# Kernel tuning notes

Hardware: AMD Instinct MI355X
Metric: run time of the kernel (lower is better)

Reference implementation:

```python
import jax, jax.numpy as jnp
import numpy as np

B, I, H, OH = 16384, 256, 256, 64
N_STEPS = 8  # fixed-step dopri5 (adaptive step control replaced by fixed grid for jit)


def setup_inputs() -> dict:
    key = jax.random.key(0)
    ks = jax.random.split(key, 12)
    sH = 1.0 / np.sqrt(H)
    sOH = 1.0 / np.sqrt(OH)
    u = lambda k, shape, s: jax.random.uniform(k, shape, jnp.float32, -s, s)
    return {
        "input": jax.random.normal(ks[0], (B, I), jnp.float32),
        "h_prev": jax.random.normal(ks[1], (B, H), jnp.float32),
        "c_prev": jax.random.normal(ks[2], (B, H), jnp.float32),
        "timespans": jax.random.uniform(ks[3], (B,), jnp.float32, 0.05, 1.0),
        # LSTMCell params (PyTorch layout: gates stacked as [i, f, g, o])
        "W_ih": u(ks[4], (4 * H, I), sH),
        "W_hh": u(ks[5], (4 * H, H), sH),
        "b_ih": u(ks[6], (4 * H,), sH),
        "b_hh": u(ks[7], (4 * H,), sH),
        # ode_func: Linear(H, OH) -> Tanh -> Linear(OH, H)
        "W1": u(ks[8], (OH, H), sH),
        "b1": u(ks[9], (OH,), sH),
        "W2": u(ks[10], (H, OH), sOH),
        "b2": u(ks[11], (H,), sOH),
    }


def reference(input, h_prev, c_prev, timespans, W_ih, W_hh, b_ih, b_hh, W1, b1, W2, b2):
    # --- LSTMCell ---
    gates = input @ W_ih.T + b_ih + h_prev @ W_hh.T + b_hh  # (B, 4H)
    gi, gf, gg, go = jnp.split(gates, 4, axis=-1)
    i = jax.nn.sigmoid(gi)
    f = jax.nn.sigmoid(gf)
    g = jnp.tanh(gg)
    o = jax.nn.sigmoid(go)
    c = f * c_prev + i * g
    h = o * jnp.tanh(c)

    # --- Neural ODE: dy/dt = MLP(y), autonomous, Dormand-Prince RK45 ---
    def ode_f(y):
        return jnp.tanh(y @ W1.T + b1) @ W2.T + b2

    dt = (timespans / N_STEPS)[:, None]  # (B, 1) per-sample step size

    def dopri5_step(y, _):
        k1 = ode_f(y)
        k2 = ode_f(y + dt * (1.0 / 5.0 * k1))
        k3 = ode_f(y + dt * (3.0 / 40.0 * k1 + 9.0 / 40.0 * k2))
        k4 = ode_f(y + dt * (44.0 / 45.0 * k1 - 56.0 / 15.0 * k2 + 32.0 / 9.0 * k3))
        k5 = ode_f(y + dt * (19372.0 / 6561.0 * k1 - 25360.0 / 2187.0 * k2
                             + 64448.0 / 6561.0 * k3 - 212.0 / 729.0 * k4))
        k6 = ode_f(y + dt * (9017.0 / 3168.0 * k1 - 355.0 / 33.0 * k2
                             + 46732.0 / 5247.0 * k3 + 49.0 / 176.0 * k4
                             - 5103.0 / 18656.0 * k5))
        y_next = y + dt * (35.0 / 384.0 * k1 + 500.0 / 1113.0 * k3 + 125.0 / 192.0 * k4
                           - 2187.0 / 6784.0 * k5 + 11.0 / 84.0 * k6)
        return y_next, None

    h_ode, _ = jax.lax.scan(dopri5_step, h, None, length=N_STEPS)
    return h_ode, c
```

## Files before the change

kernel.cpp:

```cpp
#include <hip/hip_runtime.h>
#include <hip/hip_bf16.h>


#define B_N 16384
#define H_N 256

typedef __attribute__((ext_vector_type(8))) short short8;
typedef __attribute__((ext_vector_type(4))) unsigned short u16x4;
typedef __attribute__((ext_vector_type(4))) float f32x4;

__device__ __forceinline__ unsigned short f2bf_s(float x) {
  __hip_bfloat16 h = __float2bfloat16(x);
  return *reinterpret_cast<unsigned short*>(&h);
}

__device__ __forceinline__ short8 pack8f(const float* p) {
  const f32x4 a = *(const f32x4*)p;
  const f32x4 b = *(const f32x4*)(p + 4);
  short8 r;
  r[0] = (short)f2bf_s(a[0]); r[1] = (short)f2bf_s(a[1]);
  r[2] = (short)f2bf_s(a[2]); r[3] = (short)f2bf_s(a[3]);
  r[4] = (short)f2bf_s(b[0]); r[5] = (short)f2bf_s(b[1]);
  r[6] = (short)f2bf_s(b[2]); r[7] = (short)f2bf_s(b[3]);
  return r;
}

__device__ __forceinline__ u16x4 pack4(f32x4 v) {
  u16x4 r;
  r[0] = f2bf_s(v[0]); r[1] = f2bf_s(v[1]);
  r[2] = f2bf_s(v[2]); r[3] = f2bf_s(v[3]);
  return r;
}

__device__ __forceinline__ float fast_sigmoid(float x) {
  return __builtin_amdgcn_rcpf(1.f + __expf(-x));
}
__device__ __forceinline__ float fast_tanh(float x) {
  x = fminf(15.f, fmaxf(-15.f, x));
  float e = __expf(2.f * x);
  return 1.f - 2.f * __builtin_amdgcn_rcpf(e + 1.f);
}

__device__ __forceinline__ void gl_lds16(const void* g, void* l) {
  __builtin_amdgcn_global_load_lds(
      (const __attribute__((address_space(1))) void*)g,
      (__attribute__((address_space(3))) void*)l, 16, 0, 0);
}

__global__ __launch_bounds__(256) void prep_kernel(
    const float* __restrict__ Wih, const float* __restrict__ Whh,
    const float* __restrict__ W1, const float* __restrict__ W2,
    const float* __restrict__ b2,
    unsigned short* __restrict__ wsB, unsigned short* __restrict__ wcB,
    float* __restrict__ uF) {
  const int bx = blockIdx.x;
  if (bx < 256) {
    int idx = bx * 256 + threadIdx.x;
    int n = idx >> 6, c = idx & 63, k = c * 8;
    const float* src = (k < 256) ? (Wih + (size_t)n * 256 + k)
                                 : (Whh + (size_t)n * 256 + (k - 256));
    *(short8*)(wsB + (size_t)n * 512 + k) = pack8f(src);
  } else if (bx < 272) {
    int idx = (bx - 256) * 256 + threadIdx.x;
    int f = idx >> 6, o = idx & 63;
    float acc = 0.f;
    for (int h = 0; h < 256; ++h)
      acc = fmaf(W1[f * 256 + h], W2[h * 64 + o], acc);
    wcB[f * 64 + o] = f2bf_s(acc);
  } else {
    int f = threadIdx.x;
    if (f < 64) {
      float acc = 0.f;
      for (int h = 0; h < 256; ++h) acc = fmaf(W1[f * 256 + h], b2[h], acc);
      uF[f] = acc;
    }
  }
}

__global__ __launch_bounds__(256, 2) void lstm_kernel(
    const float* __restrict__ x, const float* __restrict__ hp,
    const float* __restrict__ cp, const unsigned short* __restrict__ wsB,
    const float* __restrict__ bih, const float* __restrict__ bhh,
    float* __restrict__ out) {
  __shared__ __align__(16) float As[128 * 64];
  __shared__ __align__(16) unsigned short Bs[256 * 64];

  const int lane = threadIdx.x & 63;
  const int wv = threadIdx.x >> 6;
  const int s = lane & 15, q = lane >> 4;
  const int mb = blockIdx.x * 128;
  const int hb = blockIdx.y * 64;

  f32x4 acc[2][16];
#pragma unroll
  for (int mt = 0; mt < 2; ++mt)
#pragma unroll
    for (int tn = 0; tn < 16; ++tn) acc[mt][tn] = (f32x4){0.f, 0.f, 0.f, 0.f};

  float bsum[16];
#pragma unroll
  for (int tn = 0; tn < 16; ++tn) {
    int n = (tn >> 2) * 256 + hb + (tn & 3) * 16 + s;
    bsum[tn] = bih[n] + bhh[n];
  }

  for (int kt8 = 0; kt8 < 8; ++kt8) {
    const int k0 = kt8 * 64;
    if (kt8) __syncthreads();
    {
      const float* srcA = (k0 < 256) ? x : hp;
      const int kl = k0 & 255;
#pragma unroll
      for (int c = 0; c < 8; ++c) {
        int row = (wv * 8 + c) * 4 + (lane >> 4);
        int uc = (lane & 15) ^ (row & 15);
        gl_lds16(srcA + (size_t)(mb + row) * 256 + kl + uc * 4,
                 (char*)As + (wv * 8 + c) * 1024);
      }
    }
#pragma unroll
    for (int c = 0; c < 8; ++c) {
      int t = (wv * 8 + c) * 8 + (lane >> 3);
      int uc = (lane & 7) ^ (t & 7);
      int gr = (t >> 6) * 256 + hb + (t & 63);
      gl_lds16(wsB + (size_t)gr * 512 + k0 + uc * 8,
               (char*)Bs + (wv * 8 + c) * 1024);
    }
    __syncthreads();

#pragma unroll
    for (int kk = 0; kk < 2; ++kk) {
      short8 af[2];
#pragma unroll
      for (int mt = 0; mt < 2; ++mt) {
        int ar = wv * 32 + mt * 16 + s;
        int c0 = kk * 8 + q * 2;
        float tmp[8];
        *(f32x4*)tmp = *(const f32x4*)((char*)As + ar * 256 + ((c0 ^ (ar & 15)) * 16));
        *(f32x4*)(tmp + 4) =
            *(const f32x4*)((char*)As + ar * 256 + (((c0 + 1) ^ (ar & 15)) * 16));
        af[mt] = pack8f(tmp);
      }
#pragma unroll
      for (int tn = 0; tn < 16; ++tn) {
        int t = (tn >> 2) * 64 + (tn & 3) * 16 + s;
        int ch = (kk * 4 + q) ^ (t & 7);
        short8 bf = *(const short8*)((char*)Bs + t * 128 + ch * 16);
        acc[0][tn] = __builtin_amdgcn_mfma_f32_16x16x32_bf16(af[0], bf, acc[0][tn], 0, 0, 0);
        acc[1][tn] = __builtin_amdgcn_mfma_f32_16x16x32_bf16(af[1], bf, acc[1][tn], 0, 0, 0);
      }
    }
  }

#pragma unroll
  for (int mt = 0; mt < 2; ++mt)
#pragma unroll
    for (int ntl = 0; ntl < 4; ++ntl)
#pragma unroll
      for (int r = 0; r < 4; ++r) {
        int sample = mb + wv * 32 + mt * 16 + q * 4 + r;
        int h = hb + ntl * 16 + s;
        float gi = acc[mt][ntl][r]      + bsum[ntl];
        float gf = acc[mt][4 + ntl][r]  + bsum[4 + ntl];
        float gg = acc[mt][8 + ntl][r]  + bsum[8 + ntl];
        float go = acc[mt][12 + ntl][r] + bsum[12 + ntl];
        float iv = fast_sigmoid(gi), fv = fast_sigmoid(gf);
        float gv = fast_tanh(gg), ov = fast_sigmoid(go);
        float c = fv * cp[(size_t)sample * 256 + h] + iv * gv;
        float hv = ov * fast_tanh(c);
        out[(size_t)B_N * H_N + (size_t)sample * 256 + h] = c;
        out[(size_t)sample * 256 + h] = hv;
      }
}

__global__ __launch_bounds__(256, 4) void ode_kernel(
    float* __restrict__ out, const float* __restrict__ ts,
    const float* __restrict__ W1, const unsigned short* __restrict__ wcB,
    const float* __restrict__ uF, const float* __restrict__ W2,
    const float* __restrict__ b1, const float* __restrict__ b2) {
  __shared__ __align__(16) unsigned short zcA[16 * 64];
  __shared__ __align__(16) unsigned short zcB2[16 * 64];
  char* zA = (char*)zcA;
  char* zB = (char*)zcB2;

  const int tid = threadIdx.x;
  const int lane = tid & 63, wv = tid >> 6;
  const int s = lane & 15, q = lane >> 4;
  const int bb = blockIdx.x * 16;
  const int sx7 = s & 7;

  short8 wcf[2];
#pragma unroll
  for (int kt = 0; kt < 2; ++kt)
    wcf[kt] = *(const short8*)(wcB + (size_t)(wv * 16 + s) * 64 + kt * 32 + q * 8);

  const f32x4 b1v = *(const f32x4*)(b1 + wv * 16 + q * 4);
  const f32x4 u4 = *(const f32x4*)(uF + wv * 16 + q * 4);
  const float dt = ts[bb + s] * 0.125f;

  f32x4 yreg[4];
#pragma unroll
  for (int i = 0; i < 4; ++i)
    yreg[i] = *(const f32x4*)(out + (size_t)(bb + s) * 256 + wv * 64 + i * 16 + q * 4);

  f32x4 G = (f32x4){0.f, 0.f, 0.f, 0.f};
#pragma unroll
  for (int kt = 0; kt < 8; ++kt) {
    short8 w1f = pack8f(W1 + (size_t)(wv * 16 + s) * 256 + kt * 32 + q * 8);
    short8 yf = pack8f(out + (size_t)(bb + s) * 256 + kt * 32 + q * 8);
    G = __builtin_amdgcn_mfma_f32_16x16x32_bf16(w1f, yf, G, 0, 0, 0);
  }

  const int zwoff = (((wv * 2 + (q >> 1)) ^ sx7) << 4) + (q & 1) * 8;
  const int rb = s * 128;

  auto stz = [&](char* buf, f32x4 v) { *(u16x4*)(buf + rb + zwoff) = pack4(v); };
  auto wcmm = [&](const char* buf) -> f32x4 {
    const char* rp = buf + rb;
    short8 zf0 = *(const short8*)(rp + ((q ^ sx7) << 4));
    short8 zf1 = *(const short8*)(rp + (((4 + q) ^ sx7) << 4));
    f32x4 a = (f32x4){0.f, 0.f, 0.f, 0.f};
    a = __builtin_amdgcn_mfma_f32_16x16x32_bf16(wcf[0], zf0, a, 0, 0, 0);
    a = __builtin_amdgcn_mfma_f32_16x16x32_bf16(wcf[1], zf1, a, 0, 0, 0);
    return a;
  };
  auto stage = [&](char* buf, f32x4 zc, float cj) -> f32x4 {
    stz(buf, zc);
    __syncthreads();
    f32x4 o = wcmm(buf);
    f32x4 zo;
#pragma unroll
    for (int r = 0; r < 4; ++r)
      zo[r] = fast_tanh(fmaf(dt, fmaf(cj, u4[r], o[r]), G[r]) + b1v[r]);
    return zo;
  };

  const float A31 = 3.f / 40.f, A32 = 9.f / 40.f;
  const float A41 = 44.f / 45.f, A42 = -56.f / 15.f, A43 = 32.f / 9.f;
  const float A51 = 19372.f / 6561.f, A52 = -25360.f / 2187.f,
              A53 = 64448.f / 6561.f, A54 = -212.f / 729.f;
  const float A61 = 9017.f / 3168.f, A62 = -355.f / 33.f, A63 = 46732.f / 5247.f,
              A64 = 49.f / 176.f, A65 = -5103.f / 18656.f;
  const float C1 = 35.f / 384.f, C3 = 500.f / 1113.f, C4 = 125.f / 192.f,
              C5 = -2187.f / 6784.f, C6 = 11.f / 84.f;

  f32x4 SC = (f32x4){0.f, 0.f, 0.f, 0.f};

  for (int st = 0; st < 8; ++st) {
    f32x4 z1;
#pragma unroll
    for (int r = 0; r < 4; ++r) z1[r] = fast_tanh(G[r] + b1v[r]);

    f32x4 z2 = stage(zA, 0.2f * z1, 0.2f);
    f32x4 z3 = stage(zB, A31 * z1 + A32 * z2, 0.3f);
    f32x4 z4 = stage(zA, A41 * z1 + A42 * z2 + A43 * z3, 0.8f);
    f32x4 z5 = stage(zB, A51 * z1 + A52 * z2 + A53 * z3 + A54 * z4, 8.f / 9.f);
    f32x4 z6 = stage(zA, A61 * z1 + A62 * z2 + A63 * z3 + A64 * z4 + A65 * z5, 1.0f);

    f32x4 zc = C1 * z1 + C3 * z3 + C4 * z4 + C5 * z5 + C6 * z6;
    stz(zB, zc);
    __syncthreads();
    f32x4 o6 = wcmm(zB);
    SC += zc;
#pragma unroll
    for (int r = 0; r < 4; ++r) G[r] = fmaf(dt, u4[r] + o6[r], G[r]);
  }

  stz(zA, SC);
  __syncthreads();
  {
    const char* rp = zA + rb;
    short8 zf0 = *(const short8*)(rp + ((q ^ sx7) << 4));
    short8 zf1 = *(const short8*)(rp + (((4 + q) ^ sx7) << 4));
#pragma unroll
    for (int i = 0; i < 4; ++i) {
      short8 w2f0 = pack8f(W2 + (size_t)(wv * 64 + i * 16 + s) * 64 + q * 8);
      short8 w2f1 = pack8f(W2 + (size_t)(wv * 64 + i * 16 + s) * 64 + 32 + q * 8);
      f32x4 a = (f32x4){0.f, 0.f, 0.f, 0.f};
      a = __builtin_amdgcn_mfma_f32_16x16x32_bf16(w2f0, zf0, a, 0, 0, 0);
      a = __builtin_amdgcn_mfma_f32_16x16x32_bf16(w2f1, zf1, a, 0, 0, 0);
      f32x4 b2v = *(const f32x4*)(b2 + wv * 64 + i * 16 + q * 4);
#pragma unroll
      for (int r = 0; r < 4; ++r)
        yreg[i][r] = fmaf(dt, fmaf(8.f, b2v[r], a[r]), yreg[i][r]);
    }
  }

#pragma unroll
  for (int i = 0; i < 4; ++i)
    *(f32x4*)(out + (size_t)(bb + s) * 256 + wv * 64 + i * 16 + q * 4) = yreg[i];
}

extern "C" void kernel_launch(void* const* d_in, const int* in_sizes, int n_in,
                              void* d_out, int out_size, void* d_ws, size_t ws_size,
                              hipStream_t stream) {
  const float* x   = (const float*)d_in[0];
  const float* hp  = (const float*)d_in[1];
  const float* cp  = (const float*)d_in[2];
  const float* ts  = (const float*)d_in[3];
  const float* Wih = (const float*)d_in[4];
  const float* Whh = (const float*)d_in[5];
  const float* bih = (const float*)d_in[6];
  const float* bhh = (const float*)d_in[7];
  const float* W1  = (const float*)d_in[8];
  const float* b1  = (const float*)d_in[9];
  const float* W2  = (const float*)d_in[10];
  const float* b2  = (const float*)d_in[11];
  float* out = (float*)d_out;

  unsigned short* wsB = (unsigned short*)d_ws;
  unsigned short* wcB = wsB + 1024 * 512;
  float* uF = (float*)((char*)d_ws + 1024 * 1024 + 8192);

  prep_kernel<<<273, 256, 0, stream>>>(Wih, Whh, W1, W2, b2, wsB, wcB, uF);
  lstm_kernel<<<dim3(128, 4), 256, 0, stream>>>(x, hp, cp, wsB, bih, bhh, out);
  ode_kernel<<<1024, 256, 0, stream>>>(out, ts, W1, wcB, uF, W2, b1, b2);
}
```

Before: 90.34 us.

## Double-buffer LSTM GEMM staging with 8 waves and split prep reductions

Rewrites the LSTM GEMM kernel to use 512 threads (8 waves in a 4x2 row/column grid), a K-tile of 32, and double-buffered LDS. The next tile is staged while the current one is computed, so global-to-LDS loads overlap the MFMAs instead of sitting behind a barrier. Per-wave accumulators drop from 32 to 16 tiles, which lowers register pressure so more waves can be resident. The prep reductions are split into four independent FMA chains to shorten dependency latency. In exchange there are more barriers per K step (16 instead of 8), and the bias values are now loaded per element in the epilogue rather than preloaded.

```diff
diff --git a/kernel.cpp b/kernel.cpp
--- a/kernel.cpp
+++ b/kernel.cpp
@@ -63,107 +63,115 @@
   } else if (bx < 272) {
     int idx = (bx - 256) * 256 + threadIdx.x;
     int f = idx >> 6, o = idx & 63;
-    float acc = 0.f;
-    for (int h = 0; h < 256; ++h)
-      acc = fmaf(W1[f * 256 + h], W2[h * 64 + o], acc);
-    wcB[f * 64 + o] = f2bf_s(acc);
+    float a0 = 0.f, a1 = 0.f, a2 = 0.f, a3 = 0.f;
+    for (int h = 0; h < 256; h += 4) {
+      a0 = fmaf(W1[f * 256 + h],     W2[h * 64 + o],        a0);
+      a1 = fmaf(W1[f * 256 + h + 1], W2[(h + 1) * 64 + o],  a1);
+      a2 = fmaf(W1[f * 256 + h + 2], W2[(h + 2) * 64 + o],  a2);
+      a3 = fmaf(W1[f * 256 + h + 3], W2[(h + 3) * 64 + o],  a3);
+    }
+    wcB[f * 64 + o] = f2bf_s((a0 + a1) + (a2 + a3));
   } else {
     int f = threadIdx.x;
     if (f < 64) {
-      float acc = 0.f;
-      for (int h = 0; h < 256; ++h) acc = fmaf(W1[f * 256 + h], b2[h], acc);
-      uF[f] = acc;
-    }
-  }
-}
-
-__global__ __launch_bounds__(256, 2) void lstm_kernel(
+      float a0 = 0.f, a1 = 0.f, a2 = 0.f, a3 = 0.f;
+      for (int h = 0; h < 256; h += 4) {
+        a0 = fmaf(W1[f * 256 + h],     b2[h],     a0);
+        a1 = fmaf(W1[f * 256 + h + 1], b2[h + 1], a1);
+        a2 = fmaf(W1[f * 256 + h + 2], b2[h + 2], a2);
+        a3 = fmaf(W1[f * 256 + h + 3], b2[h + 3], a3);
+      }
+      uF[f] = (a0 + a1) + (a2 + a3);
+    }
+  }
+}
+
+__global__ __launch_bounds__(512, 4) void lstm_kernel(
     const float* __restrict__ x, const float* __restrict__ hp,
     const float* __restrict__ cp, const unsigned short* __restrict__ wsB,
     const float* __restrict__ bih, const float* __restrict__ bhh,
     float* __restrict__ out) {
-  __shared__ __align__(16) float As[128 * 64];
-  __shared__ __align__(16) unsigned short Bs[256 * 64];
-
-  const int lane = threadIdx.x & 63;
-  const int wv = threadIdx.x >> 6;
+  __shared__ __align__(16) float As2[2][128 * 32];
+  __shared__ __align__(16) unsigned short Bs2[2][256 * 32];
+
+  const int tid = threadIdx.x;
+  const int lane = tid & 63;
+  const int wv = tid >> 6;
+  const int rg = wv >> 1;
+  const int cg = wv & 1;
   const int s = lane & 15, q = lane >> 4;
   const int mb = blockIdx.x * 128;
   const int hb = blockIdx.y * 64;
 
-  f32x4 acc[2][16];
+  f32x4 acc[2][8];
 #pragma unroll
   for (int mt = 0; mt < 2; ++mt)
 #pragma unroll
-    for (int tn = 0; tn < 16; ++tn) acc[mt][tn] = (f32x4){0.f, 0.f, 0.f, 0.f};
-
-  float bsum[16];
-#pragma unroll
-  for (int tn = 0; tn < 16; ++tn) {
-    int n = (tn >> 2) * 256 + hb + (tn & 3) * 16 + s;
-    bsum[tn] = bih[n] + bhh[n];
-  }
-
-  for (int kt8 = 0; kt8 < 8; ++kt8) {
-    const int k0 = kt8 * 64;
-    if (kt8) __syncthreads();
-    {
-      const float* srcA = (k0 < 256) ? x : hp;
-      const int kl = k0 & 255;
-#pragma unroll
-      for (int c = 0; c < 8; ++c) {
-        int row = (wv * 8 + c) * 4 + (lane >> 4);
-        int uc = (lane & 15) ^ (row & 15);
-        gl_lds16(srcA + (size_t)(mb + row) * 256 + kl + uc * 4,
-                 (char*)As + (wv * 8 + c) * 1024);
-      }
-    }
-#pragma unroll
-    for (int c = 0; c < 8; ++c) {
-      int t = (wv * 8 + c) * 8 + (lane >> 3);
-      int uc = (lane & 7) ^ (t & 7);
-      int gr = (t >> 6) * 256 + hb + (t & 63);
-      gl_lds16(wsB + (size_t)gr * 512 + k0 + uc * 8,
-               (char*)Bs + (wv * 8 + c) * 1024);
+    for (int tn = 0; tn < 8; ++tn) acc[mt][tn] = (f32x4){0.f, 0.f, 0.f, 0.f};
+
+  const int c16a = wv * 2;
+  const int rowA0 = c16a * 8 + (lane >> 3);
+  const int gcA = (lane & 7) ^ (rowA0 & 7);
+  const int rowB0 = c16a * 16 + (lane >> 2);
+  const int rowB1 = rowB0 + 16;
+  const int gcB0 = (lane & 3) ^ ((rowB0 >> 1) & 3);
+  const int gcB1 = (lane & 3) ^ ((rowB1 >> 1) & 3);
+  const int grB0 = (rowB0 >> 6) * 256 + hb + (rowB0 & 63);
+  const int grB1 = (rowB1 >> 6) * 256 + hb + (rowB1 & 63);
+
+  auto STAGE = [&](int buf, int kt) {
+    const float* srcA = (kt < 8) ? x : hp;
+    const int kl = (kt * 32) & 255;
+    gl_lds16(srcA + (size_t)(mb + rowA0) * 256 + kl + gcA * 4,
+             (char*)As2[buf] + c16a * 1024);
+    gl_lds16(srcA + (size_t)(mb + rowA0 + 8) * 256 + kl + gcA * 4,
+             (char*)As2[buf] + (c16a + 1) * 1024);
+    gl_lds16(wsB + (size_t)grB0 * 512 + kt * 32 + gcB0 * 8,
+             (char*)Bs2[buf] + c16a * 1024);
+    gl_lds16(wsB + (size_t)grB1 * 512 + kt * 32 + gcB1 * 8,
+             (char*)Bs2[buf] + (c16a + 1) * 1024);
+  };
+
+  STAGE(0, 0);
+  __syncthreads();
+
+  for (int kt = 0; kt < 16; ++kt) {
+    const int buf = kt & 1;
+    if (kt < 15) STAGE(buf ^ 1, kt + 1);
+
+    short8 af[2];
+#pragma unroll
+    for (int mt = 0; mt < 2; ++mt) {
+      const int ar = rg * 32 + mt * 16 + s;
+      const char* ap = (const char*)As2[buf] + ar * 128;
+      float tmp[8];
+      *(f32x4*)tmp = *(const f32x4*)(ap + (((q * 2) ^ (ar & 7)) << 4));
+      *(f32x4*)(tmp + 4) = *(const f32x4*)(ap + (((q * 2 + 1) ^ (ar & 7)) << 4));
+      af[mt] = pack8f(tmp);
+    }
+    const char* bp = (const char*)Bs2[buf];
+#pragma unroll
+    for (int tn = 0; tn < 8; ++tn) {
+      const int t = (tn >> 1) * 64 + cg * 32 + (tn & 1) * 16 + s;
+      short8 bfr = *(const short8*)(bp + t * 64 + ((q ^ ((t >> 1) & 3)) << 4));
+      acc[0][tn] = __builtin_amdgcn_mfma_f32_16x16x32_bf16(af[0], bfr, acc[0][tn], 0, 0, 0);
+      acc[1][tn] = __builtin_amdgcn_mfma_f32_16x16x32_bf16(af[1], bfr, acc[1][tn], 0, 0, 0);
     }
     __syncthreads();
-
-#pragma unroll
-    for (int kk = 0; kk < 2; ++kk) {
-      short8 af[2];
-#pragma unroll
-      for (int mt = 0; mt < 2; ++mt) {
-        int ar = wv * 32 + mt * 16 + s;
-        int c0 = kk * 8 + q * 2;
-        float tmp[8];
-        *(f32x4*)tmp = *(const f32x4*)((char*)As + ar * 256 + ((c0 ^ (ar & 15)) * 16));
-        *(f32x4*)(tmp + 4) =
-            *(const f32x4*)((char*)As + ar * 256 + (((c0 + 1) ^ (ar & 15)) * 16));
-        af[mt] = pack8f(tmp);
-      }
-#pragma unroll
-      for (int tn = 0; tn < 16; ++tn) {
-        int t = (tn >> 2) * 64 + (tn & 3) * 16 + s;
-        int ch = (kk * 4 + q) ^ (t & 7);
-        short8 bf = *(const short8*)((char*)Bs + t * 128 + ch * 16);
-        acc[0][tn] = __builtin_amdgcn_mfma_f32_16x16x32_bf16(af[0], bf, acc[0][tn], 0, 0, 0);
-        acc[1][tn] = __builtin_amdgcn_mfma_f32_16x16x32_bf16(af[1], bf, acc[1][tn], 0, 0, 0);
-      }
-    }
   }
 
 #pragma unroll
   for (int mt = 0; mt < 2; ++mt)
 #pragma unroll
-    for (int ntl = 0; ntl < 4; ++ntl)
+    for (int ntl = 0; ntl < 2; ++ntl)
 #pragma unroll
       for (int r = 0; r < 4; ++r) {
-        int sample = mb + wv * 32 + mt * 16 + q * 4 + r;
-        int h = hb + ntl * 16 + s;
-        float gi = acc[mt][ntl][r]      + bsum[ntl];
-        float gf = acc[mt][4 + ntl][r]  + bsum[4 + ntl];
-        float gg = acc[mt][8 + ntl][r]  + bsum[8 + ntl];
-        float go = acc[mt][12 + ntl][r] + bsum[12 + ntl];
+        int sample = mb + rg * 32 + mt * 16 + q * 4 + r;
+        int h = hb + cg * 32 + ntl * 16 + s;
+        float gi = acc[mt][0 + ntl][r] + bih[h] + bhh[h];
+        float gf = acc[mt][2 + ntl][r] + bih[256 + h] + bhh[256 + h];
+        float gg = acc[mt][4 + ntl][r] + bih[512 + h] + bhh[512 + h];
+        float go = acc[mt][6 + ntl][r] + bih[768 + h] + bhh[768 + h];
         float iv = fast_sigmoid(gi), fv = fast_sigmoid(gf);
         float gv = fast_tanh(gg), ov = fast_sigmoid(go);
         float c = fv * cp[(size_t)sample * 256 + h] + iv * gv;
@@ -313,6 +321,6 @@
   float* uF = (float*)((char*)d_ws + 1024 * 1024 + 8192);
 
   prep_kernel<<<273, 256, 0, stream>>>(Wih, Whh, W1, W2, b2, wsB, wcB, uF);
-  lstm_kernel<<<dim3(128, 4), 256, 0, stream>>>(x, hp, cp, wsB, bih, bhh, out);
+  lstm_kernel<<<dim3(128, 4), 512, 0, stream>>>(x, hp, cp, wsB, bih, bhh, out);
   ode_kernel<<<1024, 256, 0, stream>>>(out, ts, W1, wcB, uF, W2, b1, b2);
 }
```

New measurement: 79.05 us. 1.14x faster.
